# Kernel tuning notes

Measured on AMD Instinct MI355X. Metric: run time of the kernel, lower is better.

Reference implementation:

```python
import jax, jax.numpy as jnp
import numpy as np

D = 1024  # dim_context


def setup_inputs() -> dict:
    key = jax.random.key(0)
    k1, k2, k3, k4, k5 = jax.random.split(key, 5)
    B, T = 32, 2048
    hidden = jax.random.normal(k1, (B, D), dtype=jnp.float32)
    encoder_outputs = jax.random.normal(k2, (B, T, D), dtype=jnp.float32)
    # nn.Linear(2D, D): weight [D, 2D], bias [D]
    lim = 1.0 / np.sqrt(2 * D)
    W = jax.random.uniform(k3, (D, 2 * D), minval=-lim, maxval=lim, dtype=jnp.float32)
    b = jax.random.uniform(k4, (D,), minval=-lim, maxval=lim, dtype=jnp.float32)
    stdv = 1.0 / np.sqrt(D)
    v = jax.random.uniform(k5, (D,), minval=-stdv, maxval=stdv, dtype=jnp.float32)
    return {"hidden": hidden, "encoder_outputs": encoder_outputs, "W": W, "b": b, "v": v}


def reference(hidden, encoder_outputs, W, b, v):
    # hidden: [B, D]; encoder_outputs: [B, T, D]
    B, T, Dm = encoder_outputs.shape
    h = jnp.broadcast_to(hidden[:, None, :], (B, T, Dm))      # repeat over T
    attn_inputs = jnp.concatenate([h, encoder_outputs], axis=2)  # [B, T, 2D]
    energy = jax.nn.relu(jnp.einsum('btk,dk->btd', attn_inputs, W) + b)  # [B, T, D]
    scores = jnp.einsum('btd,d->bt', energy, v)                # [B, T]
    # softmax over dim=1 (time axis), then unsqueeze(1)
    return jax.nn.softmax(scores, axis=1)[:, None, :]          # [B, 1, T]
```

## Files before the change

kernel.cpp:

```cpp
#include <hip/hip_runtime.h>
#include <cstdint>


#define GLOBAL_AS __attribute__((address_space(1)))
#define LDS_AS    __attribute__((address_space(3)))

typedef __bf16 bf16x8 __attribute__((ext_vector_type(8)));
typedef float  f32x4  __attribute__((ext_vector_type(4)));

__device__ __forceinline__ unsigned int f2bf(float x) {
    unsigned int u = __builtin_bit_cast(unsigned int, x);
    u += 0x7fffu + ((u >> 16) & 1u);
    return u >> 16;
}

__device__ __forceinline__ uint4 pack8(float4 f0, float4 f1) {
    uint4 o;
    o.x = f2bf(f0.x) | (f2bf(f0.y) << 16);
    o.y = f2bf(f0.z) | (f2bf(f0.w) << 16);
    o.z = f2bf(f1.x) | (f2bf(f1.y) << 16);
    o.w = f2bf(f1.z) | (f2bf(f1.w) << 16);
    return o;
}

__global__ __launch_bounds__(256) void k_convert_we(const float* __restrict__ W,
                                                    uint2* __restrict__ out) {
    int idx = blockIdx.x * 256 + threadIdx.x;
    int i = idx * 4;
    int n = i >> 10, k = i & 1023;
    const float4 f = *(const float4*)(W + (size_t)n * 2048 + 1024 + k);
    uint2 o;
    o.x = f2bf(f.x) | (f2bf(f.y) << 16);
    o.y = f2bf(f.z) | (f2bf(f.w) << 16);
    out[idx] = o;
}

__global__ __launch_bounds__(256) void k_hidden_proj(const float* __restrict__ hidden,
                                                     const float* __restrict__ W,
                                                     const float* __restrict__ bias,
                                                     float* __restrict__ u) {
    __shared__ float wrow[1024];
    __shared__ float red[256];
    const int tid = threadIdx.x, d = blockIdx.x;
    ((float4*)wrow)[tid] = ((const float4*)(W + (size_t)d * 2048))[tid];
    __syncthreads();
    const int b = tid & 31, kc = tid >> 5;
    const float* h = hidden + b * 1024 + kc * 128;
    const float* w = wrow + kc * 128;
    float acc = 0.f;
    #pragma unroll 8
    for (int i = 0; i < 128; i += 4) {
        float4 hv = *(const float4*)(h + i);
        acc += w[i] * hv.x + w[i + 1] * hv.y + w[i + 2] * hv.z + w[i + 3] * hv.w;
    }
    red[tid] = acc;
    __syncthreads();
    if (tid < 32) {
        float s = 0.f;
        #pragma unroll
        for (int j = 0; j < 8; j++) s += red[j * 32 + tid];
        u[tid * 1024 + d] = s + bias[d];
    }
}

__global__ __launch_bounds__(256) void k_gemm_score(
        const float* __restrict__ Af,
        unsigned short* __restrict__ Ab,
        const unsigned short* __restrict__ Bw,
        const float* __restrict__ u,
        const float* __restrict__ v,
        float* __restrict__ scores) {
    constexpr int K = 1024, BK = 32;
    __shared__ __align__(16) unsigned short As[128 * BK];
    __shared__ __align__(16) unsigned short Bs[128 * BK];
    __shared__ float red[2][128];

    const int tid  = threadIdx.x;
    const int wave = tid >> 6;
    const int lane = tid & 63;
    const int mb   = blockIdx.x;
    const int wm = wave & 1, wn = wave >> 1;
    const int q = lane >> 4, cl = lane & 15;

    int aoff[4], boff[4];
    #pragma unroll
    for (int i = 0; i < 4; i++) {
        int ra = wm * 64 + i * 16 + cl;
        aoff[i] = ra * BK + (q ^ ((ra >> 1) & 3)) * 8;
        int rb = wn * 64 + i * 16 + cl;
        boff[i] = rb * BK + (q ^ ((rb >> 1) & 3)) * 8;
    }

    const int rl  = lane >> 2;
    const int kbs = lane & 3;
    int srow[2], skb[2];
    #pragma unroll
    for (int c = 0; c < 2; c++) {
        int chunk = wave * 2 + c;
        srow[c] = chunk * 16 + rl;
        skb[c]  = kbs ^ ((srow[c] >> 1) & 3);
    }

    float sacc[4][4];
    #pragma unroll
    for (int i = 0; i < 4; i++)
        #pragma unroll
        for (int r = 0; r < 4; r++) sacc[i][r] = 0.f;

    const int bidx = mb >> 4;
    f32x4 acc[4][4];

    for (int nb = 0; nb < 8; nb++) {
        #pragma unroll
        for (int i = 0; i < 4; i++)
            #pragma unroll
            for (int j = 0; j < 4; j++) acc[i][j] = (f32x4){0.f, 0.f, 0.f, 0.f};

        for (int k0 = 0; k0 < K; k0 += BK) {
            if (nb == 0) {
                #pragma unroll
                for (int c = 0; c < 2; c++) {
                    const int chunk = wave * 2 + c;
                    const size_t aidx = (size_t)(mb * 128 + srow[c]) * K + k0 + skb[c] * 8;
                    const float4* gs = (const float4*)(Af + aidx);
                    uint4 o = pack8(gs[0], gs[1]);
                    *(uint4*)(As + chunk * 512 + lane * 8) = o;
                    *(uint4*)(Ab + aidx) = o;
                    const unsigned short* gb = Bw + (size_t)srow[c] * K + k0 + skb[c] * 8;
                    __builtin_amdgcn_global_load_lds((GLOBAL_AS void*)(size_t)gb,
                                                     (LDS_AS void*)(Bs + chunk * 512), 16, 0, 0);
                }
            } else {
                #pragma unroll
                for (int c = 0; c < 2; c++) {
                    const int chunk = wave * 2 + c;
                    const unsigned short* ga = Ab + (size_t)(mb * 128 + srow[c]) * K + k0 + skb[c] * 8;
                    const unsigned short* gb = Bw + (size_t)(nb * 128 + srow[c]) * K + k0 + skb[c] * 8;
                    __builtin_amdgcn_global_load_lds((GLOBAL_AS void*)(size_t)ga,
                                                     (LDS_AS void*)(As + chunk * 512), 16, 0, 0);
                    __builtin_amdgcn_global_load_lds((GLOBAL_AS void*)(size_t)gb,
                                                     (LDS_AS void*)(Bs + chunk * 512), 16, 0, 0);
                }
            }
            __syncthreads();
            bf16x8 afr[4], bfr[4];
            #pragma unroll
            for (int i = 0; i < 4; i++) afr[i] = *(const bf16x8*)(As + aoff[i]);
            #pragma unroll
            for (int j = 0; j < 4; j++) bfr[j] = *(const bf16x8*)(Bs + boff[j]);
            #pragma unroll
            for (int i = 0; i < 4; i++)
                #pragma unroll
                for (int j = 0; j < 4; j++)
                    acc[i][j] = __builtin_amdgcn_mfma_f32_16x16x32_bf16(afr[i], bfr[j], acc[i][j], 0, 0, 0);
            __syncthreads();
        }

        float vv[4], uu[4];
        #pragma unroll
        for (int j = 0; j < 4; j++) {
            int n = nb * 128 + wn * 64 + j * 16 + cl;
            vv[j] = v[n];
            uu[j] = u[bidx * 1024 + n];
        }
        #pragma unroll
        for (int i = 0; i < 4; i++)
            #pragma unroll
            for (int r = 0; r < 4; r++) {
                float s = sacc[i][r];
                #pragma unroll
                for (int j = 0; j < 4; j++)
                    s += fmaxf(acc[i][j][r] + uu[j], 0.f) * vv[j];
                sacc[i][r] = s;
            }
    }

    #pragma unroll
    for (int i = 0; i < 4; i++)
        #pragma unroll
        for (int r = 0; r < 4; r++) {
            float s = sacc[i][r];
            s += __shfl_xor(s, 1);
            s += __shfl_xor(s, 2);
            s += __shfl_xor(s, 4);
            s += __shfl_xor(s, 8);
            if (cl == 0) red[wn][wm * 64 + i * 16 + q * 4 + r] = s;
        }
    __syncthreads();
    if (tid < 128) scores[mb * 128 + tid] = red[0][tid] + red[1][tid];
}

__global__ __launch_bounds__(256) void k_softmax(const float* __restrict__ scores,
                                                 float* __restrict__ out) {
    __shared__ float red[4];
    int b = blockIdx.x;
    int t0 = threadIdx.x;
    int wave = threadIdx.x >> 6, lane = threadIdx.x & 63;
    const float* s = scores + b * 2048;
    float vals[8];
    float lmax = -1e30f;
    #pragma unroll
    for (int i = 0; i < 8; i++) {
        vals[i] = s[t0 + i * 256];
        lmax = fmaxf(lmax, vals[i]);
    }
    for (int o = 32; o > 0; o >>= 1) lmax = fmaxf(lmax, __shfl_xor(lmax, o));
    if (lane == 0) red[wave] = lmax;
    __syncthreads();
    float gmax = fmaxf(fmaxf(red[0], red[1]), fmaxf(red[2], red[3]));
    float lsum = 0.f;
    #pragma unroll
    for (int i = 0; i < 8; i++) {
        vals[i] = expf(vals[i] - gmax);
        lsum += vals[i];
    }
    for (int o = 32; o > 0; o >>= 1) lsum += __shfl_xor(lsum, o);
    __syncthreads();
    if (lane == 0) red[wave] = lsum;
    __syncthreads();
    float inv = 1.0f / (red[0] + red[1] + red[2] + red[3]);
    #pragma unroll
    for (int i = 0; i < 8; i++) out[b * 2048 + t0 + i * 256] = vals[i] * inv;
}

extern "C" void kernel_launch(void* const* d_in, const int* in_sizes, int n_in,
                              void* d_out, int out_size, void* d_ws, size_t ws_size,
                              hipStream_t stream) {
    const float* hidden = (const float*)d_in[0];
    const float* enc    = (const float*)d_in[1];
    const float* W      = (const float*)d_in[2];
    const float* bias   = (const float*)d_in[3];
    const float* v      = (const float*)d_in[4];
    float* out = (float*)d_out;

    char* ws = (char*)d_ws;
    unsigned short* encb = (unsigned short*)ws;
    unsigned short* Web  = (unsigned short*)(ws + 134217728);
    float* u      = (float*)(ws + 134217728 + 2097152);
    float* scores = (float*)(ws + 134217728 + 2097152 + 131072);

    k_hidden_proj<<<1024, 256, 0, stream>>>(hidden, W, bias, u);
    k_convert_we<<<1024, 256, 0, stream>>>(W, (uint2*)Web);
    k_gemm_score<<<512, 256, 0, stream>>>(enc, encb, Web, u, v, scores);
    k_softmax<<<32, 256, 0, stream>>>(scores, out);
}
```

Measured before the change: 625.6 us.

## Split GEMM N across two grid slices, pre-convert encoder to bf16, widen BK

Moves the fp32-to-bf16 conversion of encoder outputs into a separate streaming kernel, so the GEMM loads only bf16 through global_load_lds. It splits the N dimension across blockIdx.y (2 slices of 4 column tiles) to double the block count to 1024. It also raises BK to 64 with a new XOR swizzle. Partial scores from each slice go to separate buffers and are summed in softmax. This trades an extra full pass over the encoder tensor and reloading A twice for more parallelism and fewer barriers per K step.

After: 559.5 us. -10.6%, faster.

```diff
diff --git a/kernel.cpp b/kernel.cpp
--- a/kernel.cpp
+++ b/kernel.cpp
@@ -14,13 +14,17 @@
     return u >> 16;
 }
 
-__device__ __forceinline__ uint4 pack8(float4 f0, float4 f1) {
+__global__ __launch_bounds__(256) void k_convert_enc(const float4* __restrict__ in,
+                                                     uint4* __restrict__ out) {
+    size_t idx = (size_t)blockIdx.x * 256 + threadIdx.x;
+    float4 f0 = in[idx * 2];
+    float4 f1 = in[idx * 2 + 1];
     uint4 o;
     o.x = f2bf(f0.x) | (f2bf(f0.y) << 16);
     o.y = f2bf(f0.z) | (f2bf(f0.w) << 16);
     o.z = f2bf(f1.x) | (f2bf(f1.y) << 16);
     o.w = f2bf(f1.z) | (f2bf(f1.w) << 16);
-    return o;
+    out[idx] = o;
 }
 
 __global__ __launch_bounds__(256) void k_convert_we(const float* __restrict__ W,
@@ -63,14 +67,13 @@
     }
 }
 
-__global__ __launch_bounds__(256) void k_gemm_score(
-        const float* __restrict__ Af,
-        unsigned short* __restrict__ Ab,
+__global__ __launch_bounds__(256, 4) void k_gemm_score(
+        const unsigned short* __restrict__ Ab,
         const unsigned short* __restrict__ Bw,
         const float* __restrict__ u,
         const float* __restrict__ v,
-        float* __restrict__ scores) {
-    constexpr int K = 1024, BK = 32;
+        float* __restrict__ scores2) {
+    constexpr int K = 1024, BK = 64;
     __shared__ __align__(16) unsigned short As[128 * BK];
     __shared__ __align__(16) unsigned short Bs[128 * BK];
     __shared__ float red[2][128];
@@ -79,6 +82,7 @@
     const int wave = tid >> 6;
     const int lane = tid & 63;
     const int mb   = blockIdx.x;
+    const int z    = blockIdx.y;
     const int wm = wave & 1, wn = wave >> 1;
     const int q = lane >> 4, cl = lane & 15;
 
@@ -86,20 +90,19 @@
     #pragma unroll
     for (int i = 0; i < 4; i++) {
         int ra = wm * 64 + i * 16 + cl;
-        aoff[i] = ra * BK + (q ^ ((ra >> 1) & 3)) * 8;
+        aoff[i] = ra * 64 + ((q ^ (ra & 7)) << 3);
         int rb = wn * 64 + i * 16 + cl;
-        boff[i] = rb * BK + (q ^ ((rb >> 1) & 3)) * 8;
-    }
-
-    const int rl  = lane >> 2;
-    const int kbs = lane & 3;
-    int srow[2], skb[2];
-    #pragma unroll
-    for (int c = 0; c < 2; c++) {
-        int chunk = wave * 2 + c;
-        srow[c] = chunk * 16 + rl;
-        skb[c]  = kbs ^ ((srow[c] >> 1) & 3);
-    }
+        boff[i] = rb * 64 + ((q ^ (rb & 7)) << 3);
+    }
+
+    int soff[4];
+    #pragma unroll
+    for (int c = 0; c < 4; c++) {
+        int row = (wave * 4 + c) * 8 + (lane >> 3);
+        int g   = (lane & 7) ^ (row & 7);
+        soff[c] = row * K + g * 8;
+    }
+    const unsigned short* Abase = Ab + (size_t)(mb * 128) * K;
 
     float sacc[4][4];
     #pragma unroll
@@ -110,49 +113,40 @@
     const int bidx = mb >> 4;
     f32x4 acc[4][4];
 
-    for (int nb = 0; nb < 8; nb++) {
+    for (int p = 0; p < 4; p++) {
+        const int nb = z * 4 + p;
+        const unsigned short* Bbase = Bw + (size_t)(nb * 128) * K;
         #pragma unroll
         for (int i = 0; i < 4; i++)
             #pragma unroll
             for (int j = 0; j < 4; j++) acc[i][j] = (f32x4){0.f, 0.f, 0.f, 0.f};
 
         for (int k0 = 0; k0 < K; k0 += BK) {
-            if (nb == 0) {
-                #pragma unroll
-                for (int c = 0; c < 2; c++) {
-                    const int chunk = wave * 2 + c;
-                    const size_t aidx = (size_t)(mb * 128 + srow[c]) * K + k0 + skb[c] * 8;
-                    const float4* gs = (const float4*)(Af + aidx);
-                    uint4 o = pack8(gs[0], gs[1]);
-                    *(uint4*)(As + chunk * 512 + lane * 8) = o;
-                    *(uint4*)(Ab + aidx) = o;
-                    const unsigned short* gb = Bw + (size_t)srow[c] * K + k0 + skb[c] * 8;
-                    __builtin_amdgcn_global_load_lds((GLOBAL_AS void*)(size_t)gb,
-                                                     (LDS_AS void*)(Bs + chunk * 512), 16, 0, 0);
-                }
-            } else {
-                #pragma unroll
-                for (int c = 0; c < 2; c++) {
-                    const int chunk = wave * 2 + c;
-                    const unsigned short* ga = Ab + (size_t)(mb * 128 + srow[c]) * K + k0 + skb[c] * 8;
-                    const unsigned short* gb = Bw + (size_t)(nb * 128 + srow[c]) * K + k0 + skb[c] * 8;
-                    __builtin_amdgcn_global_load_lds((GLOBAL_AS void*)(size_t)ga,
-                                                     (LDS_AS void*)(As + chunk * 512), 16, 0, 0);
-                    __builtin_amdgcn_global_load_lds((GLOBAL_AS void*)(size_t)gb,
-                                                     (LDS_AS void*)(Bs + chunk * 512), 16, 0, 0);
-                }
+            #pragma unroll
+            for (int c = 0; c < 4; c++) {
+                const int chunk = wave * 4 + c;
+                __builtin_amdgcn_global_load_lds(
+                    (GLOBAL_AS void*)(size_t)(Abase + soff[c] + k0),
+                    (LDS_AS void*)(As + chunk * 512), 16, 0, 0);
+                __builtin_amdgcn_global_load_lds(
+                    (GLOBAL_AS void*)(size_t)(Bbase + soff[c] + k0),
+                    (LDS_AS void*)(Bs + chunk * 512), 16, 0, 0);
             }
             __syncthreads();
-            bf16x8 afr[4], bfr[4];
-            #pragma unroll
-            for (int i = 0; i < 4; i++) afr[i] = *(const bf16x8*)(As + aoff[i]);
-            #pragma unroll
-            for (int j = 0; j < 4; j++) bfr[j] = *(const bf16x8*)(Bs + boff[j]);
-            #pragma unroll
-            for (int i = 0; i < 4; i++)
-                #pragma unroll
-                for (int j = 0; j < 4; j++)
-                    acc[i][j] = __builtin_amdgcn_mfma_f32_16x16x32_bf16(afr[i], bfr[j], acc[i][j], 0, 0, 0);
+            #pragma unroll
+            for (int h = 0; h < 2; h++) {
+                const int hx = h * 32;
+                bf16x8 afr[4], bfr[4];
+                #pragma unroll
+                for (int i = 0; i < 4; i++) afr[i] = *(const bf16x8*)(As + (aoff[i] ^ hx));
+                #pragma unroll
+                for (int j = 0; j < 4; j++) bfr[j] = *(const bf16x8*)(Bs + (boff[j] ^ hx));
+                #pragma unroll
+                for (int i = 0; i < 4; i++)
+                    #pragma unroll
+                    for (int j = 0; j < 4; j++)
+                        acc[i][j] = __builtin_amdgcn_mfma_f32_16x16x32_bf16(afr[i], bfr[j], acc[i][j], 0, 0, 0);
+            }
             __syncthreads();
         }
 
@@ -187,21 +181,23 @@
             if (cl == 0) red[wn][wm * 64 + i * 16 + q * 4 + r] = s;
         }
     __syncthreads();
-    if (tid < 128) scores[mb * 128 + tid] = red[0][tid] + red[1][tid];
-}
-
-__global__ __launch_bounds__(256) void k_softmax(const float* __restrict__ scores,
+    if (tid < 128) scores2[(size_t)z * 65536 + mb * 128 + tid] = red[0][tid] + red[1][tid];
+}
+
+__global__ __launch_bounds__(256) void k_softmax(const float* __restrict__ scores2,
                                                  float* __restrict__ out) {
     __shared__ float red[4];
     int b = blockIdx.x;
     int t0 = threadIdx.x;
     int wave = threadIdx.x >> 6, lane = threadIdx.x & 63;
-    const float* s = scores + b * 2048;
+    const float* s0 = scores2 + b * 2048;
+    const float* s1 = scores2 + 65536 + b * 2048;
     float vals[8];
     float lmax = -1e30f;
     #pragma unroll
     for (int i = 0; i < 8; i++) {
-        vals[i] = s[t0 + i * 256];
+        int t = t0 + i * 256;
+        vals[i] = s0[t] + s1[t];
         lmax = fmaxf(lmax, vals[i]);
     }
     for (int o = 32; o > 0; o >>= 1) lmax = fmaxf(lmax, __shfl_xor(lmax, o));
@@ -236,11 +232,13 @@
     char* ws = (char*)d_ws;
     unsigned short* encb = (unsigned short*)ws;
     unsigned short* Web  = (unsigned short*)(ws + 134217728);
-    float* u      = (float*)(ws + 134217728 + 2097152);
-    float* scores = (float*)(ws + 134217728 + 2097152 + 131072);
-
+    float* u       = (float*)(ws + 134217728 + 2097152);
+    float* scores2 = (float*)(ws + 134217728 + 2097152 + 131072);
+
+    k_convert_enc<<<32768, 256, 0, stream>>>((const float4*)enc, (uint4*)encb);
+    k_convert_we<<<1024, 256, 0, stream>>>(W, (uint2*)Web);
     k_hidden_proj<<<1024, 256, 0, stream>>>(hidden, W, bias, u);
-    k_convert_we<<<1024, 256, 0, stream>>>(W, (uint2*)Web);
-    k_gemm_score<<<512, 256, 0, stream>>>(enc, encb, Web, u, v, scores);
-    k_softmax<<<32, 256, 0, stream>>>(scores, out);
-}
+    dim3 g(512, 2);
+    k_gemm_score<<<g, 256, 0, stream>>>(encb, Web, u, v, scores2);
+    k_softmax<<<32, 256, 0, stream>>>(scores2, out);
+}
```
